# Kernel tuning notes

Measured on AMD Instinct MI355X. Metric: run time of the kernel, lower is better.

## Reference

```python
import jax, jax.numpy as jnp
import numpy as np

N = 8192
NHID = 256

def setup_inputs() -> dict:
    key = jax.random.key(0)
    ks = jax.random.split(key, 9)
    s = 1.0 / np.sqrt(NHID)  # torch Linear default init scale
    return {
        "x1": jax.random.normal(ks[0], (N, NHID), jnp.float32),
        "x2": jax.random.normal(ks[1], (N, NHID), jnp.float32),
        "x3": jax.random.normal(ks[2], (N, NHID), jnp.float32),
        "Wq": jax.random.uniform(ks[3], (NHID, NHID), jnp.float32, -s, s),
        "bq": jax.random.uniform(ks[4], (NHID,), jnp.float32, -s, s),
        "Wk": jax.random.uniform(ks[5], (NHID, NHID), jnp.float32, -s, s),
        "bk": jax.random.uniform(ks[6], (NHID,), jnp.float32, -s, s),
        "Wv": jax.random.uniform(ks[7], (NHID, NHID), jnp.float32, -s, s),
        "bv": jax.random.uniform(ks[8], (NHID,), jnp.float32, -s, s),
    }

def reference(x1, x2, x3, Wq, bq, Wk, bk, Wv, bv):
    # torch.nn.Linear: y = x @ W.T + b
    q = x1 @ Wq.T + bq                      # [N, nhid]
    k = x2 @ Wk.T + bk                      # [N, nhid]
    v = x3 @ Wv.T + bv                      # [N, nhid]
    scores = q @ k.T                        # [N, N], NOTE: unscaled (no 1/sqrt(d))
    attn = jax.nn.softmax(scores, axis=1)   # softmax over keys (dim=1)
    return attn @ v                         # [N, nhid]
```

## Files before the change

kernel.cpp:

```cpp
#include <hip/hip_runtime.h>
#include <stdint.h>

typedef unsigned short u16;
typedef __attribute__((ext_vector_type(8))) short short8;
typedef __attribute__((ext_vector_type(4))) float f32x4;

#define LOG2E 1.4426950408889634f
#define NT 8192
#define DH 256
#define NSP 8

#define QH     0
#define KH     2097152
#define VTB    4194304
#define OPARTB 6291456
#define XH0 6291456
#define XL0 8388608
#define XH1 10485760
#define XL1 12582912
#define XH2 14680064
#define XL2 16777216
#define WQH 18874368
#define WQL 18939904
#define WKH 19005440
#define WKL 19070976
#define WVH 19136512
#define WVL 19202048
#define MPART_F 11534336
#define LPART_F 11599872

__device__ __forceinline__ u16 f2bf(float f) {
  union { float f; uint32_t u; } c; c.f = f;
  uint32_t u = c.u;
  return (u16)((u + 0x7fffu + ((u >> 16) & 1)) >> 16);
}
__device__ __forceinline__ u16 f2bf_hu(float f) {
  union { float f; uint32_t u; } c; c.f = f;
  return (u16)((c.u + 0x8000u) >> 16);
}
__device__ __forceinline__ float bf2f(u16 h) {
  union { uint32_t u; float f; } c; c.u = ((uint32_t)h) << 16;
  return c.f;
}

__device__ __forceinline__ int swz32(int u, int row) {
  return (u & 24) | ((u & 7) ^ (row & 7));
}

__device__ __forceinline__ f32x4 mfma16(short8 a, short8 b, f32x4 c) {
  return __builtin_amdgcn_mfma_f32_16x16x32_bf16(a, b, c, 0, 0, 0);
}

__device__ __forceinline__ void gl_lds16(const u16* g, u16* l) {
  __builtin_amdgcn_global_load_lds(
      (const __attribute__((address_space(1))) uint32_t*)g,
      (__attribute__((address_space(3))) uint32_t*)l, 16, 0, 0);
}

__global__ __launch_bounds__(256) void k_convert(
    const float* __restrict__ x1, const float* __restrict__ x2, const float* __restrict__ x3,
    const float* __restrict__ wq, const float* __restrict__ wk, const float* __restrict__ wv,
    u16* __restrict__ wsu) {
  int b = blockIdx.x;
  const float* src; u16 *dh, *dl; int bl;
  if (b < 1024)      { src = x1; dh = wsu + XH0; dl = wsu + XL0; bl = b; }
  else if (b < 2048) { src = x2; dh = wsu + XH1; dl = wsu + XL1; bl = b - 1024; }
  else if (b < 3072) { src = x3; dh = wsu + XH2; dl = wsu + XL2; bl = b - 2048; }
  else if (b < 3104) { src = wq; dh = wsu + WQH; dl = wsu + WQL; bl = b - 3072; }
  else if (b < 3136) { src = wk; dh = wsu + WKH; dl = wsu + WKL; bl = b - 3104; }
  else               { src = wv; dh = wsu + WVH; dl = wsu + WVL; bl = b - 3136; }
  int i = (bl * 256 + threadIdx.x) * 8;
  f32x4 a = *(const f32x4*)(src + i);
  f32x4 c = *(const f32x4*)(src + i + 4);
  short8 rh, rl;
  float v[8] = {a[0], a[1], a[2], a[3], c[0], c[1], c[2], c[3]};
#pragma unroll
  for (int j = 0; j < 8; j++) {
    u16 h = f2bf(v[j]);
    rh[j] = (short)h;
    rl[j] = (short)f2bf(v[j] - bf2f(h));
  }
  *(short8*)(dh + i) = rh;
  *(short8*)(dl + i) = rl;
}

__global__ __launch_bounds__(256) void k_qkv(
    u16* __restrict__ wsu,
    const float* __restrict__ bq, const float* __restrict__ bk, const float* __restrict__ bv) {
  __shared__ u16 sAh[64 * 256];
  __shared__ u16 sAl[64 * 256];
  __shared__ u16 sBh[32 * 256];
  __shared__ u16 sBl[32 * 256];
  int bx = blockIdx.x;
  int mid = bx >> 10;
  int t = bx & 1023;
  const u16 *Ah, *Al, *Bh, *Bl; u16 *Ohi; const float* bias;
  int rb, cb, ldO, biasRow;
  if (mid == 0) {
    Ah = wsu + XH0; Al = wsu + XL0; Bh = wsu + WQH; Bl = wsu + WQL;
    Ohi = wsu + QH; bias = bq; biasRow = 0; ldO = 256;
    rb = t >> 3; cb = t & 7;
  } else if (mid == 1) {
    Ah = wsu + XH1; Al = wsu + XL1; Bh = wsu + WKH; Bl = wsu + WKL;
    Ohi = wsu + KH; bias = bk; biasRow = 0; ldO = 256;
    rb = t >> 3; cb = t & 7;
  } else {
    Ah = wsu + WVH; Al = wsu + WVL; Bh = wsu + XH2; Bl = wsu + XL2;
    Ohi = wsu + VTB; bias = bv; biasRow = 1; ldO = 8192;
    rb = t >> 8; cb = t & 255;
  }

  int tid = threadIdx.x;
#pragma unroll
  for (int i = 0; i < 8; i++) {
    int L = i * 256 + tid;
    int row = L >> 5, u = L & 31;
    short8 vh = *(const short8*)(Ah + (rb * 64 + row) * 256 + u * 8);
    short8 vl = *(const short8*)(Al + (rb * 64 + row) * 256 + u * 8);
    *(short8*)(&sAh[row * 256 + swz32(u, row) * 8]) = vh;
    *(short8*)(&sAl[row * 256 + swz32(u, row) * 8]) = vl;
  }
#pragma unroll
  for (int i = 0; i < 4; i++) {
    int L = i * 256 + tid;
    int row = L >> 5, u = L & 31;
    short8 vh = *(const short8*)(Bh + (cb * 32 + row) * 256 + u * 8);
    short8 vl = *(const short8*)(Bl + (cb * 32 + row) * 256 + u * 8);
    *(short8*)(&sBh[row * 256 + swz32(u, row) * 8]) = vh;
    *(short8*)(&sBl[row * 256 + swz32(u, row) * 8]) = vl;
  }
  __syncthreads();

  int lane = tid & 63, wave = tid >> 6;
  int n = lane & 15, quad = lane >> 4;
  int wm = wave >> 1, wn = wave & 1;
  f32x4 acc0 = {0.f,0.f,0.f,0.f}, acc1 = {0.f,0.f,0.f,0.f};
#pragma unroll
  for (int kk = 0; kk < 8; kk++) {
    int ra = wm * 32 + n;
    int sa0 = ra * 256 + swz32(kk * 4 + quad, ra) * 8;
    int sa1 = (ra + 16) * 256 + swz32(kk * 4 + quad, ra + 16) * 8;
    short8 a0h = *(const short8*)(&sAh[sa0]);
    short8 a1h = *(const short8*)(&sAh[sa1]);
    short8 a0l = *(const short8*)(&sAl[sa0]);
    short8 a1l = *(const short8*)(&sAl[sa1]);
    int rbB = wn * 16 + n;
    int sb = rbB * 256 + swz32(kk * 4 + quad, rbB) * 8;
    short8 bh = *(const short8*)(&sBh[sb]);
    short8 bl = *(const short8*)(&sBl[sb]);
    acc0 = mfma16(a0h, bh, acc0);
    acc1 = mfma16(a1h, bh, acc1);
    acc0 = mfma16(a0h, bl, acc0);
    acc1 = mfma16(a1h, bl, acc1);
    acc0 = mfma16(a0l, bh, acc0);
    acc1 = mfma16(a1l, bh, acc1);
  }
  int colg = cb * 32 + wn * 16 + n;
  float bcol = biasRow ? 0.0f : bias[colg];
#pragma unroll
  for (int mt = 0; mt < 2; mt++) {
    f32x4 acc = mt ? acc1 : acc0;
#pragma unroll
    for (int r = 0; r < 4; r++) {
      int rowg = rb * 64 + wm * 32 + mt * 16 + quad * 4 + r;
      float bb = biasRow ? bias[rowg] : bcol;
      Ohi[rowg * ldO + colg] = f2bf(acc[r] + bb);
    }
  }
}

__global__ __launch_bounds__(256, 2) void k_flash(
    const u16* __restrict__ wsu, u16* __restrict__ opart, float* __restrict__ wsf) {
  __shared__ u16 sK[2][32 * 256];
  __shared__ u16 sV[2][256 * 32];
  __shared__ u16 sP[4 * 32 * 40];

  int qb = blockIdx.x >> 3, sp = blockIdx.x & 7;
  int tid = threadIdx.x, lane = tid & 63, wave = tid >> 6;
  int n = lane & 15, quad = lane >> 4;
  const u16* Qp = wsu + QH;
  const u16* Kp = wsu + KH;
  const u16* Vp = wsu + VTB;

  short8 qf[2][8];
  int rowQ0 = qb * 128 + wave * 32 + n;
#pragma unroll
  for (int mt = 0; mt < 2; mt++)
#pragma unroll
    for (int kk = 0; kk < 8; kk++)
      qf[mt][kk] = *(const short8*)(Qp + (size_t)(rowQ0 + mt * 16) * 256 + kk * 32 + quad * 8);

  int krow_base = wave * 2 + (lane >> 5);
  int kgu = (lane & 24) | ((lane & 7) ^ (krow_base & 7));
  int vd_base = wave * 16 + (lane >> 2);
  int vgu = (lane & 3) ^ ((lane >> 3) & 3);

  int key00 = sp * 1024;

#pragma unroll
  for (int i = 0; i < 4; i++) {
    gl_lds16(Kp + (size_t)(key00 + i * 8 + krow_base) * 256 + kgu * 8,
             &sK[0][i * 2048 + wave * 512]);
    gl_lds16(Vp + (size_t)(i * 64 + vd_base) * 8192 + key00 + vgu * 8,
             &sV[0][i * 2048 + wave * 512]);
  }

  f32x4 o[2][16];
#pragma unroll
  for (int mt = 0; mt < 2; mt++)
#pragma unroll
    for (int nt = 0; nt < 16; nt++) { o[mt][nt][0]=0.f; o[mt][nt][1]=0.f; o[mt][nt][2]=0.f; o[mt][nt][3]=0.f; }
  float negm0L[8], lcur[8];
#pragma unroll
  for (int j = 0; j < 8; j++) { negm0L[j] = 0.f; lcur[j] = 0.f; }

  for (int it = 0; it < 32; it++) {
    __syncthreads();
    int cur = it & 1;
    if (it + 1 < 32) {
      int k1 = key00 + (it + 1) * 32;
#pragma unroll
      for (int i = 0; i < 4; i++) {
        gl_lds16(Kp + (size_t)(k1 + i * 8 + krow_base) * 256 + kgu * 8,
                 &sK[cur ^ 1][i * 2048 + wave * 512]);
        gl_lds16(Vp + (size_t)(i * 64 + vd_base) * 8192 + k1 + vgu * 8,
                 &sV[cur ^ 1][i * 2048 + wave * 512]);
      }
    }
    const u16* bK = sK[cur];
    const u16* bV = sV[cur];

    f32x4 s[2][2];
#pragma unroll
    for (int mt = 0; mt < 2; mt++)
#pragma unroll
      for (int ntk = 0; ntk < 2; ntk++) { s[mt][ntk][0]=0.f; s[mt][ntk][1]=0.f; s[mt][ntk][2]=0.f; s[mt][ntk][3]=0.f; }
#pragma unroll
    for (int kk = 0; kk < 8; kk++) {
      int su = swz32(kk * 4 + quad, n) * 8;
      short8 b0 = *(const short8*)(&bK[n * 256 + su]);
      short8 b1 = *(const short8*)(&bK[(n + 16) * 256 + su]);
      s[0][0] = mfma16(qf[0][kk], b0, s[0][0]);
      s[0][1] = mfma16(qf[0][kk], b1, s[0][1]);
      s[1][0] = mfma16(qf[1][kk], b0, s[1][0]);
      s[1][1] = mfma16(qf[1][kk], b1, s[1][1]);
    }

    if (it == 0) {
#pragma unroll
      for (int mt = 0; mt < 2; mt++)
#pragma unroll
        for (int r = 0; r < 4; r++) {
          float v = fmaxf(s[mt][0][r], s[mt][1][r]);
          v = fmaxf(v, __shfl_xor(v, 1));
          v = fmaxf(v, __shfl_xor(v, 2));
          v = fmaxf(v, __shfl_xor(v, 4));
          v = fmaxf(v, __shfl_xor(v, 8));
          negm0L[mt * 4 + r] = -v * LOG2E;
        }
    }

    u16* myP = &sP[wave * 1280];
#pragma unroll
    for (int mt = 0; mt < 2; mt++)
#pragma unroll
      for (int r = 0; r < 4; r++) {
        int j = mt * 4 + r;
        float x0 = fminf(fmaf(s[mt][0][r], LOG2E, negm0L[j]), 110.f);
        float x1 = fminf(fmaf(s[mt][1][r], LOG2E, negm0L[j]), 110.f);
        float p0 = exp2f(x0);
        float p1 = exp2f(x1);
        lcur[j] += p0 + p1;
        int row = mt * 16 + quad * 4 + r;
        myP[row * 40 + n] = f2bf_hu(p0);
        myP[row * 40 + 16 + n] = f2bf_hu(p1);
      }

    short8 pa0 = *(const short8*)(&myP[n * 40 + quad * 8]);
    short8 pa1 = *(const short8*)(&myP[(16 + n) * 40 + quad * 8]);
#pragma unroll
    for (int nt = 0; nt < 16; nt++) {
      int d = nt * 16 + n;
      short8 vb = *(const short8*)(&bV[d * 32 + (quad ^ ((n >> 1) & 3)) * 8]);
      o[0][nt] = mfma16(pa0, vb, o[0][nt]);
      o[1][nt] = mfma16(pa1, vb, o[1][nt]);
    }
  }

#pragma unroll
  for (int j = 0; j < 8; j++) {
    float v = lcur[j];
    v += __shfl_xor(v, 1); v += __shfl_xor(v, 2);
    v += __shfl_xor(v, 4); v += __shfl_xor(v, 8);
    lcur[j] = v;
  }

  u16* op = opart + (size_t)sp * (NT * DH);
  int rowb = qb * 128 + wave * 32;
#pragma unroll
  for (int mt = 0; mt < 2; mt++)
#pragma unroll
    for (int nt = 0; nt < 16; nt++)
#pragma unroll
      for (int r = 0; r < 4; r++) {
        int row = rowb + mt * 16 + quad * 4 + r;
        op[(size_t)row * 256 + nt * 16 + n] = f2bf(o[mt][nt][r]);
      }
  if (n == 0) {
#pragma unroll
    for (int j = 0; j < 8; j++) {
      int row = rowb + (j >> 2) * 16 + quad * 4 + (j & 3);
      wsf[MPART_F + sp * NT + row] = negm0L[j] * -0.6931471805599453f;
      wsf[LPART_F + sp * NT + row] = lcur[j];
    }
  }
}

__global__ __launch_bounds__(256) void k_combine(
    const u16* __restrict__ opart, const float* __restrict__ wsf, float* __restrict__ out) {
  int gid = blockIdx.x * 256 + threadIdx.x;
  int row = gid >> 6, cg = gid & 63;
  float m[8], l[8];
#pragma unroll
  for (int s = 0; s < 8; s++) {
    m[s] = wsf[MPART_F + s * NT + row];
    l[s] = wsf[LPART_F + s * NT + row];
  }
  float ms = m[0];
#pragma unroll
  for (int s = 1; s < 8; s++) ms = fmaxf(ms, m[s]);
  float denom = 0.f;
  float acc[4] = {0.f, 0.f, 0.f, 0.f};
#pragma unroll
  for (int s = 0; s < 8; s++) {
    float w = exp2f((m[s] - ms) * LOG2E);
    denom += w * l[s];
    const u16* pp = opart + ((size_t)s * NT + row) * 256 + cg * 4;
    uint2 v = *(const uint2*)pp;
    acc[0] += w * bf2f((u16)(v.x & 0xffff));
    acc[1] += w * bf2f((u16)(v.x >> 16));
    acc[2] += w * bf2f((u16)(v.y & 0xffff));
    acc[3] += w * bf2f((u16)(v.y >> 16));
  }
  float inv = 1.0f / denom;
  f32x4 r = {acc[0] * inv, acc[1] * inv, acc[2] * inv, acc[3] * inv};
  *(f32x4*)(out + (size_t)row * 256 + cg * 4) = r;
}

extern "C" void kernel_launch(void* const* d_in, const int* in_sizes, int n_in,
                              void* d_out, int out_size, void* d_ws, size_t ws_size,
                              hipStream_t stream) {
  const float* x1 = (const float*)d_in[0];
  const float* x2 = (const float*)d_in[1];
  const float* x3 = (const float*)d_in[2];
  const float* Wq = (const float*)d_in[3];
  const float* bq = (const float*)d_in[4];
  const float* Wk = (const float*)d_in[5];
  const float* bk = (const float*)d_in[6];
  const float* Wv = (const float*)d_in[7];
  const float* bv = (const float*)d_in[8];
  u16* wsu = (u16*)d_ws;
  float* wsf = (float*)d_ws;
  float* out = (float*)d_out;

  k_convert<<<dim3(3168), dim3(256), 0, stream>>>(x1, x2, x3, Wq, Wk, Wv, wsu);
  k_qkv<<<dim3(3072), dim3(256), 0, stream>>>(wsu, bq, bk, bv);
  k_flash<<<dim3(512), dim3(256), 0, stream>>>(wsu, wsu + OPARTB, wsf);
  k_combine<<<dim3(2048), dim3(256), 0, stream>>>(wsu + OPARTB, wsf, out);
}
```

Measured before the change: 231.7 us.

## Stage flash K/V tiles through registers into padded LDS; drop LDS in QKV GEMM

The attention kernel no longer uses async global-to-LDS loads into swizzled buffers. Each step now loads the next K/V tile into registers, issues those loads after the QK^T MFMAs, and writes them into padded LDS (row strides 260 and 36) at the end of the step. The key loop is manually unrolled by two so the double-buffer offsets are compile-time constants. The goal is to hide load latency behind compute and simplify LDS addressing. The extra staging registers sit next to a large accumulator set under a two-blocks-per-CU bound, which risks spills or lower occupancy, and the final step prefetches a tile past the split that is never used. Separately, the QKV projection kernel drops LDS staging and feeds MFMAs directly from global memory.

```diff
diff --git a/kernel.cpp b/kernel.cpp
--- a/kernel.cpp
+++ b/kernel.cpp
@@ -8,7 +8,6 @@
 #define LOG2E 1.4426950408889634f
 #define NT 8192
 #define DH 256
-#define NSP 8
 
 #define QH     0
 #define KH     2097152
@@ -43,18 +42,8 @@
   return c.f;
 }
 
-__device__ __forceinline__ int swz32(int u, int row) {
-  return (u & 24) | ((u & 7) ^ (row & 7));
-}
-
 __device__ __forceinline__ f32x4 mfma16(short8 a, short8 b, f32x4 c) {
   return __builtin_amdgcn_mfma_f32_16x16x32_bf16(a, b, c, 0, 0, 0);
-}
-
-__device__ __forceinline__ void gl_lds16(const u16* g, u16* l) {
-  __builtin_amdgcn_global_load_lds(
-      (const __attribute__((address_space(1))) uint32_t*)g,
-      (__attribute__((address_space(3))) uint32_t*)l, 16, 0, 0);
 }
 
 __global__ __launch_bounds__(256) void k_convert(
@@ -87,67 +76,46 @@
 __global__ __launch_bounds__(256) void k_qkv(
     u16* __restrict__ wsu,
     const float* __restrict__ bq, const float* __restrict__ bk, const float* __restrict__ bv) {
-  __shared__ u16 sAh[64 * 256];
-  __shared__ u16 sAl[64 * 256];
-  __shared__ u16 sBh[32 * 256];
-  __shared__ u16 sBl[32 * 256];
   int bx = blockIdx.x;
   int mid = bx >> 10;
   int t = bx & 1023;
-  const u16 *Ah, *Al, *Bh, *Bl; u16 *Ohi; const float* bias;
+  const u16 *Ah, *Al, *Bh, *Bl; u16 *O; const float* bias;
   int rb, cb, ldO, biasRow;
   if (mid == 0) {
     Ah = wsu + XH0; Al = wsu + XL0; Bh = wsu + WQH; Bl = wsu + WQL;
-    Ohi = wsu + QH; bias = bq; biasRow = 0; ldO = 256;
+    O = wsu + QH; bias = bq; biasRow = 0; ldO = 256;
     rb = t >> 3; cb = t & 7;
   } else if (mid == 1) {
     Ah = wsu + XH1; Al = wsu + XL1; Bh = wsu + WKH; Bl = wsu + WKL;
-    Ohi = wsu + KH; bias = bk; biasRow = 0; ldO = 256;
+    O = wsu + KH; bias = bk; biasRow = 0; ldO = 256;
     rb = t >> 3; cb = t & 7;
   } else {
     Ah = wsu + WVH; Al = wsu + WVL; Bh = wsu + XH2; Bl = wsu + XL2;
-    Ohi = wsu + VTB; bias = bv; biasRow = 1; ldO = 8192;
+    O = wsu + VTB; bias = bv; biasRow = 1; ldO = 8192;
     rb = t >> 8; cb = t & 255;
   }
-
-  int tid = threadIdx.x;
-#pragma unroll
-  for (int i = 0; i < 8; i++) {
-    int L = i * 256 + tid;
-    int row = L >> 5, u = L & 31;
-    short8 vh = *(const short8*)(Ah + (rb * 64 + row) * 256 + u * 8);
-    short8 vl = *(const short8*)(Al + (rb * 64 + row) * 256 + u * 8);
-    *(short8*)(&sAh[row * 256 + swz32(u, row) * 8]) = vh;
-    *(short8*)(&sAl[row * 256 + swz32(u, row) * 8]) = vl;
-  }
-#pragma unroll
-  for (int i = 0; i < 4; i++) {
-    int L = i * 256 + tid;
-    int row = L >> 5, u = L & 31;
-    short8 vh = *(const short8*)(Bh + (cb * 32 + row) * 256 + u * 8);
-    short8 vl = *(const short8*)(Bl + (cb * 32 + row) * 256 + u * 8);
-    *(short8*)(&sBh[row * 256 + swz32(u, row) * 8]) = vh;
-    *(short8*)(&sBl[row * 256 + swz32(u, row) * 8]) = vl;
-  }
-  __syncthreads();
-
-  int lane = tid & 63, wave = tid >> 6;
+  int lane = threadIdx.x & 63, wave = threadIdx.x >> 6;
   int n = lane & 15, quad = lane >> 4;
   int wm = wave >> 1, wn = wave & 1;
+  int row0 = rb * 64 + wm * 32;
+  int col0 = cb * 32 + wn * 16;
+
+  const u16* pA0h = Ah + (size_t)(row0 + n) * 256 + quad * 8;
+  const u16* pA0l = Al + (size_t)(row0 + n) * 256 + quad * 8;
+  const u16* pA1h = pA0h + 16 * 256;
+  const u16* pA1l = pA0l + 16 * 256;
+  const u16* pBh  = Bh + (size_t)(col0 + n) * 256 + quad * 8;
+  const u16* pBl  = Bl + (size_t)(col0 + n) * 256 + quad * 8;
+
   f32x4 acc0 = {0.f,0.f,0.f,0.f}, acc1 = {0.f,0.f,0.f,0.f};
 #pragma unroll
   for (int kk = 0; kk < 8; kk++) {
-    int ra = wm * 32 + n;
-    int sa0 = ra * 256 + swz32(kk * 4 + quad, ra) * 8;
-    int sa1 = (ra + 16) * 256 + swz32(kk * 4 + quad, ra + 16) * 8;
-    short8 a0h = *(const short8*)(&sAh[sa0]);
-    short8 a1h = *(const short8*)(&sAh[sa1]);
-    short8 a0l = *(const short8*)(&sAl[sa0]);
-    short8 a1l = *(const short8*)(&sAl[sa1]);
-    int rbB = wn * 16 + n;
-    int sb = rbB * 256 + swz32(kk * 4 + quad, rbB) * 8;
-    short8 bh = *(const short8*)(&sBh[sb]);
-    short8 bl = *(const short8*)(&sBl[sb]);
+    short8 a0h = *(const short8*)(pA0h + kk * 32);
+    short8 a1h = *(const short8*)(pA1h + kk * 32);
+    short8 a0l = *(const short8*)(pA0l + kk * 32);
+    short8 a1l = *(const short8*)(pA1l + kk * 32);
+    short8 bh  = *(const short8*)(pBh + kk * 32);
+    short8 bl  = *(const short8*)(pBl + kk * 32);
     acc0 = mfma16(a0h, bh, acc0);
     acc1 = mfma16(a1h, bh, acc1);
     acc0 = mfma16(a0h, bl, acc0);
@@ -155,24 +123,28 @@
     acc0 = mfma16(a0l, bh, acc0);
     acc1 = mfma16(a1l, bh, acc1);
   }
-  int colg = cb * 32 + wn * 16 + n;
+  int colg = col0 + n;
   float bcol = biasRow ? 0.0f : bias[colg];
 #pragma unroll
   for (int mt = 0; mt < 2; mt++) {
     f32x4 acc = mt ? acc1 : acc0;
 #pragma unroll
     for (int r = 0; r < 4; r++) {
-      int rowg = rb * 64 + wm * 32 + mt * 16 + quad * 4 + r;
+      int rowg = row0 + mt * 16 + quad * 4 + r;
       float bb = biasRow ? bias[rowg] : bcol;
-      Ohi[rowg * ldO + colg] = f2bf(acc[r] + bb);
-    }
-  }
-}
-
+      O[(size_t)rowg * ldO + colg] = f2bf(acc[r] + bb);
+    }
+  }
+}
+
+#define KSTR 260
+#define VSTR 36
+#define KBUF (32 * KSTR)
+#define VBUF (256 * VSTR)
 __global__ __launch_bounds__(256, 2) void k_flash(
     const u16* __restrict__ wsu, u16* __restrict__ opart, float* __restrict__ wsf) {
-  __shared__ u16 sK[2][32 * 256];
-  __shared__ u16 sV[2][256 * 32];
+  __shared__ u16 sK[2 * KBUF];
+  __shared__ u16 sV[2 * VBUF];
   __shared__ u16 sP[4 * 32 * 40];
 
   int qb = blockIdx.x >> 3, sp = blockIdx.x & 7;
@@ -190,19 +162,27 @@
     for (int kk = 0; kk < 8; kk++)
       qf[mt][kk] = *(const short8*)(Qp + (size_t)(rowQ0 + mt * 16) * 256 + kk * 32 + quad * 8);
 
-  int krow_base = wave * 2 + (lane >> 5);
-  int kgu = (lane & 24) | ((lane & 7) ^ (krow_base & 7));
-  int vd_base = wave * 16 + (lane >> 2);
-  int vgu = (lane & 3) ^ ((lane >> 3) & 3);
-
-  int key00 = sp * 1024;
-
-#pragma unroll
-  for (int i = 0; i < 4; i++) {
-    gl_lds16(Kp + (size_t)(key00 + i * 8 + krow_base) * 256 + kgu * 8,
-             &sK[0][i * 2048 + wave * 512]);
-    gl_lds16(Vp + (size_t)(i * 64 + vd_base) * 8192 + key00 + vgu * 8,
-             &sV[0][i * 2048 + wave * 512]);
+  int kr = wave * 8 + (lane >> 3);
+  int ku = lane & 7;
+  const u16* gK = Kp + (size_t)(sp * 1024 + kr) * 256 + ku * 8;
+  u16* lK = &sK[kr * KSTR + ku * 8];
+
+  int vd = wave * 64 + (lane >> 2);
+  int vu = lane & 3;
+  const u16* gV = Vp + (size_t)vd * 8192 + sp * 1024 + vu * 8;
+  u16* lV = &sV[vd * VSTR + vu * 8];
+
+  {
+    short8 tk[4], tv[4];
+#pragma unroll
+    for (int i = 0; i < 4; i++) tk[i] = *(const short8*)(gK + i * 64);
+#pragma unroll
+    for (int i = 0; i < 4; i++) tv[i] = *(const short8*)(gV + (size_t)i * 16 * 8192);
+    gK += 32 * 256; gV += 32;
+#pragma unroll
+    for (int i = 0; i < 4; i++) *(short8*)(lK + i * 64) = tk[i];
+#pragma unroll
+    for (int i = 0; i < 4; i++) *(short8*)(lV + i * 16 * VSTR) = tv[i];
   }
 
   f32x4 o[2][16];
@@ -214,44 +194,40 @@
 #pragma unroll
   for (int j = 0; j < 8; j++) { negm0L[j] = 0.f; lcur[j] = 0.f; }
 
-  for (int it = 0; it < 32; it++) {
+  const u16* rK = &sK[n * KSTR + quad * 8];
+  const u16* rV = &sV[n * VSTR + quad * 8];
+  u16* myP = &sP[wave * 1280];
+  u16* wP  = myP + quad * 160 + n;
+  const u16* rP = &myP[n * 40 + quad * 8];
+
+  auto body = [&](int kRd, int vRd, int kWr, int vWr, bool first) {
     __syncthreads();
-    int cur = it & 1;
-    if (it + 1 < 32) {
-      int k1 = key00 + (it + 1) * 32;
-#pragma unroll
-      for (int i = 0; i < 4; i++) {
-        gl_lds16(Kp + (size_t)(k1 + i * 8 + krow_base) * 256 + kgu * 8,
-                 &sK[cur ^ 1][i * 2048 + wave * 512]);
-        gl_lds16(Vp + (size_t)(i * 64 + vd_base) * 8192 + k1 + vgu * 8,
-                 &sV[cur ^ 1][i * 2048 + wave * 512]);
-      }
-    }
-    const u16* bK = sK[cur];
-    const u16* bV = sV[cur];
-
-    f32x4 s[2][2];
-#pragma unroll
-    for (int mt = 0; mt < 2; mt++)
-#pragma unroll
-      for (int ntk = 0; ntk < 2; ntk++) { s[mt][ntk][0]=0.f; s[mt][ntk][1]=0.f; s[mt][ntk][2]=0.f; s[mt][ntk][3]=0.f; }
+
+    f32x4 s00={0.f,0.f,0.f,0.f}, s01={0.f,0.f,0.f,0.f};
+    f32x4 s10={0.f,0.f,0.f,0.f}, s11={0.f,0.f,0.f,0.f};
 #pragma unroll
     for (int kk = 0; kk < 8; kk++) {
-      int su = swz32(kk * 4 + quad, n) * 8;
-      short8 b0 = *(const short8*)(&bK[n * 256 + su]);
-      short8 b1 = *(const short8*)(&bK[(n + 16) * 256 + su]);
-      s[0][0] = mfma16(qf[0][kk], b0, s[0][0]);
-      s[0][1] = mfma16(qf[0][kk], b1, s[0][1]);
-      s[1][0] = mfma16(qf[1][kk], b0, s[1][0]);
-      s[1][1] = mfma16(qf[1][kk], b1, s[1][1]);
-    }
-
-    if (it == 0) {
+      short8 b0 = *(const short8*)(rK + kRd + kk * 32);
+      short8 b1 = *(const short8*)(rK + kRd + 16 * KSTR + kk * 32);
+      s00 = mfma16(qf[0][kk], b0, s00);
+      s01 = mfma16(qf[0][kk], b1, s01);
+      s10 = mfma16(qf[1][kk], b0, s10);
+      s11 = mfma16(qf[1][kk], b1, s11);
+    }
+
+    short8 tk[4], tv[4];
+#pragma unroll
+    for (int i = 0; i < 4; i++) tk[i] = *(const short8*)(gK + i * 64);
+#pragma unroll
+    for (int i = 0; i < 4; i++) tv[i] = *(const short8*)(gV + (size_t)i * 16 * 8192);
+    gK += 32 * 256; gV += 32;
+
+    if (first) {
 #pragma unroll
       for (int mt = 0; mt < 2; mt++)
 #pragma unroll
         for (int r = 0; r < 4; r++) {
-          float v = fmaxf(s[mt][0][r], s[mt][1][r]);
+          float v = mt ? fmaxf(s10[r], s11[r]) : fmaxf(s00[r], s01[r]);
           v = fmaxf(v, __shfl_xor(v, 1));
           v = fmaxf(v, __shfl_xor(v, 2));
           v = fmaxf(v, __shfl_xor(v, 4));
@@ -260,31 +236,41 @@
         }
     }
 
-    u16* myP = &sP[wave * 1280];
 #pragma unroll
     for (int mt = 0; mt < 2; mt++)
 #pragma unroll
       for (int r = 0; r < 4; r++) {
         int j = mt * 4 + r;
-        float x0 = fminf(fmaf(s[mt][0][r], LOG2E, negm0L[j]), 110.f);
-        float x1 = fminf(fmaf(s[mt][1][r], LOG2E, negm0L[j]), 110.f);
+        float sv0 = mt ? s10[r] : s00[r];
+        float sv1 = mt ? s11[r] : s01[r];
+        float x0 = fminf(fmaf(sv0, LOG2E, negm0L[j]), 110.f);
+        float x1 = fminf(fmaf(sv1, LOG2E, negm0L[j]), 110.f);
         float p0 = exp2f(x0);
         float p1 = exp2f(x1);
         lcur[j] += p0 + p1;
-        int row = mt * 16 + quad * 4 + r;
-        myP[row * 40 + n] = f2bf_hu(p0);
-        myP[row * 40 + 16 + n] = f2bf_hu(p1);
+        wP[(mt * 16) * 40 + r * 40]      = f2bf_hu(p0);
+        wP[(mt * 16) * 40 + r * 40 + 16] = f2bf_hu(p1);
       }
 
-    short8 pa0 = *(const short8*)(&myP[n * 40 + quad * 8]);
-    short8 pa1 = *(const short8*)(&myP[(16 + n) * 40 + quad * 8]);
+    short8 pa0 = *(const short8*)(rP);
+    short8 pa1 = *(const short8*)(rP + 640);
 #pragma unroll
     for (int nt = 0; nt < 16; nt++) {
-      int d = nt * 16 + n;
-      short8 vb = *(const short8*)(&bV[d * 32 + (quad ^ ((n >> 1) & 3)) * 8]);
+      short8 vb = *(const short8*)(rV + vRd + nt * 16 * VSTR);
       o[0][nt] = mfma16(pa0, vb, o[0][nt]);
       o[1][nt] = mfma16(pa1, vb, o[1][nt]);
     }
+
+#pragma unroll
+    for (int i = 0; i < 4; i++) *(short8*)(lK + kWr + i * 64) = tk[i];
+#pragma unroll
+    for (int i = 0; i < 4; i++) *(short8*)(lV + vWr + i * 16 * VSTR) = tv[i];
+  };
+
+#pragma unroll 1
+  for (int ii = 0; ii < 16; ii++) {
+    body(0, 0, KBUF, VBUF, ii == 0);
+    body(KBUF, VBUF, 0, 0, false);
   }
 
 #pragma unroll
```

Result: slower. 476.7 us (+105.8%).
